# Kernel optimization log

Measured on AMD Instinct MI355X. Metric: run time of the kernel, lower is better.

## Reference

```python
import jax, jax.numpy as jnp
import numpy as np

B = 128
C_IN = 1
HID = 256
LAT = 256
NC = 4096
NA = 16
G = 4
DH = 256        # DynamicsModel default hidden_dim
CE = DH // 2    # code/action embed dim
IMG = 64
COMMIT = 0.25
DN = ('NCHW', 'OIHW', 'NCHW')


def conv_s2(x, w, b):
    y = jax.lax.conv_general_dilated(x, w, (2, 2), ((1, 1), (1, 1)), dimension_numbers=DN)
    return y + b[None, :, None, None]


def deconv_s2(x, w, b):
    # torch ConvTranspose2d(k=4, s=2, p=1): flip kernel, swap I/O channels,
    wt = jnp.flip(w, (2, 3)).transpose(1, 0, 2, 3)
    y = jax.lax.conv_general_dilated(x, wt, (1, 1), ((2, 2), (2, 2)),
                                     lhs_dilation=(2, 2), dimension_numbers=DN)
    return y + b[None, :, None, None]


def setup_inputs():
    key = jax.random.key(0)
    ks = iter(jax.random.split(key, 64))

    def W(shape, fan_in):
        return jax.random.normal(next(ks), shape, jnp.float32) * np.float32(1.0 / np.sqrt(fan_in))

    inp = {}
    inp['x'] = jax.random.uniform(next(ks), (B, C_IN, IMG, IMG), jnp.float32)
    inp['x_next'] = jax.random.uniform(next(ks), (B, C_IN, IMG, IMG), jnp.float32)
    inp['action'] = jax.random.randint(next(ks), (B,), 0, NA)
    # encoder Conv2d weights: [out, in, 4, 4]
    inp['enc_w1'] = W((HID, C_IN, 4, 4), C_IN * 16); inp['enc_b1'] = jnp.zeros((HID,), jnp.float32)
    inp['enc_w2'] = W((HID, HID, 4, 4), HID * 16);   inp['enc_b2'] = jnp.zeros((HID,), jnp.float32)
    inp['enc_w3'] = W((HID, HID, 4, 4), HID * 16);   inp['enc_b3'] = jnp.zeros((HID,), jnp.float32)
    inp['enc_w4'] = W((LAT, HID, 4, 4), HID * 16);   inp['enc_b4'] = jnp.zeros((LAT,), jnp.float32)
    # decoder ConvTranspose2d weights: [in, out, 4, 4]
    inp['dec_w1'] = W((LAT, HID, 4, 4), LAT * 4);    inp['dec_b1'] = jnp.zeros((HID,), jnp.float32)
    inp['dec_w2'] = W((HID, HID, 4, 4), HID * 4);    inp['dec_b2'] = jnp.zeros((HID,), jnp.float32)
    inp['dec_w3'] = W((HID, HID, 4, 4), HID * 4);    inp['dec_b3'] = jnp.zeros((HID,), jnp.float32)
    inp['dec_w4'] = W((HID, C_IN, 4, 4), HID * 4);   inp['dec_b4'] = jnp.zeros((C_IN,), jnp.float32)
    inp['codebook'] = jax.random.normal(next(ks), (NC, LAT), jnp.float32)
    inp['code_embed'] = W((NC, CE), CE)
    inp['action_embed'] = W((NA, CE), CE)
    d_in = G * G * CE + CE
    inp['dyn_w1'] = W((d_in, DH), d_in);      inp['dyn_b1'] = jnp.zeros((DH,), jnp.float32)
    inp['dyn_w2'] = W((DH, DH), DH);          inp['dyn_b2'] = jnp.zeros((DH,), jnp.float32)
    inp['dyn_w3'] = W((DH, G * G * NC), DH);  inp['dyn_b3'] = jnp.zeros((G * G * NC,), jnp.float32)
    return inp


def reference(x, x_next, action,
              enc_w1, enc_b1, enc_w2, enc_b2, enc_w3, enc_b3, enc_w4, enc_b4,
              dec_w1, dec_b1, dec_w2, dec_b2, dec_w3, dec_b3, dec_w4, dec_b4,
              codebook, code_embed, action_embed,
              dyn_w1, dyn_b1, dyn_w2, dyn_b2, dyn_w3, dyn_b3):
    relu = jax.nn.relu
    sg = jax.lax.stop_gradient

    cb_sq = jnp.sum(codebook * codebook, axis=1)  # [NC]

    def encode(xi):
        h = relu(conv_s2(xi, enc_w1, enc_b1))
        h = relu(conv_s2(h, enc_w2, enc_b2))
        h = relu(conv_s2(h, enc_w3, enc_b3))
        z = conv_s2(h, enc_w4, enc_b4)                   # [B, LAT, G, G]
        zf = z.transpose(0, 2, 3, 1).reshape(-1, LAT)    # [B*G*G, LAT]
        # squared euclidean distances (argmin identical to cdist argmin)
        d2 = jnp.sum(zf * zf, axis=1, keepdims=True) - 2.0 * (zf @ codebook.T) + cb_sq
        codes = jnp.argmin(d2, axis=-1)                  # [B*G*G]
        zq = codebook[codes]                             # [B*G*G, LAT]
        return zf, zq, codes

    zf, zq, codes_flat = encode(x)
    commitment_loss = jnp.mean((zf - sg(zq)) ** 2)
    codebook_loss = jnp.mean((sg(zf) - zq) ** 2)
    vq_loss = codebook_loss + COMMIT * commitment_loss
    zq_st = zf + sg(zq - zf)                             # straight-through

    zq_grid = zq_st.reshape(-1, G, G, LAT).transpose(0, 3, 1, 2)  # [B, LAT, G, G]
    codes = codes_flat.reshape(-1, G, G)

    # decoder
    h = relu(deconv_s2(zq_grid, dec_w1, dec_b1))
    h = relu(deconv_s2(h, dec_w2, dec_b2))
    h = relu(deconv_s2(h, dec_w3, dec_b3))
    recon = jax.nn.sigmoid(deconv_s2(h, dec_w4, dec_b4))  # [B, 1, 64, 64]

    # dynamics
    ce = code_embed[codes].reshape(codes.shape[0], -1)    # [B, G*G*CE]
    ae = action_embed[action]                             # [B, CE]
    h2 = jnp.concatenate([ce, ae], axis=-1)
    h2 = relu(h2 @ dyn_w1 + dyn_b1)
    h2 = relu(h2 @ dyn_w2 + dyn_b2)
    next_logits = (h2 @ dyn_w3 + dyn_b3).reshape(-1, G, G, NC)

    # next-code target (no grad in original)
    _, _, nc_flat = encode(sg(x_next))
    next_codes_target = nc_flat.reshape(-1, G, G)

    return (recon, codes, commitment_loss, codebook_loss, vq_loss,
            next_logits, next_codes_target)
```

## Files before the change

### kernel.cpp

```cpp
#include <hip/hip_runtime.h>
#include <hip/hip_bf16.h>

typedef _Float16 f16;
typedef f16   f16x8 __attribute__((ext_vector_type(8)));
typedef short s16x8 __attribute__((ext_vector_type(8)));
typedef float f32x4 __attribute__((ext_vector_type(4)));
typedef unsigned short u16;

__device__ __forceinline__ f32x4 mfma_f16(f16x8 a, f16x8 b, f32x4 c){
  return __builtin_amdgcn_mfma_f32_16x16x32_f16(a,b,c,0,0,0);
}
__device__ __forceinline__ f32x4 mfma_bf16(s16x8 a, s16x8 b, f32x4 c){
  return __builtin_amdgcn_mfma_f32_16x16x32_bf16(a,b,c,0,0,0);
}
__device__ __forceinline__ u16 f2bf(float v){
  unsigned u = __float_as_uint(v);
  unsigned r = u + 0x7fffu + ((u>>16)&1u);
  return (u16)(r>>16);
}
__device__ __forceinline__ float bf2f(u16 v){ return __uint_as_float(((unsigned)v)<<16); }

#define N_B 128

#define OUT_RECON 0
#define OUT_CODES 524288
#define OUT_LC    526336
#define OUT_NL    526339
#define OUT_NCT   8914947

#define B_E1H  0ull
#define B_E1L  67108864ull
#define B_ZF   67108864ull
#define B_ZQ4  69206016ull
#define B_ZSQ  70254592ull
#define B_ACC  70287360ull
#define B_CODES 70320128ull
#define B_H1   70385664ull
#define B_H2   70516736ull
#define B_H2B  70647808ull
#define B_E3H  71303168ull
#define B_E3L  75497472ull
#define B_D1   71303168ull
#define B_D2   75497472ull
#define B_EMB  92274688ull
#define B_ZFH  100663296ull
#define B_ZFL  101711872ull
#define B_E2H  134217728ull
#define B_E2L  150994944ull
#define B_DOTS 134217728ull
#define B_WE2H 167772160ull
#define B_WE2L 169869312ull
#define B_WE3H 171966464ull
#define B_WE3L 174063616ull
#define B_WE4H 176160768ull
#define B_WE4L 178257920ull
#define B_WD1  180355072ull
#define B_WD2  182452224ull
#define B_WD3  184549376ull
#define B_CBSQ 186646528ull
#define B_ZERO 186712064ull
#define B_CBH  186712576ull
#define B_CBL  188809728ull

__global__ __launch_bounds__(256) void k_pack_enc(const float* __restrict__ w,
                                                  f16* __restrict__ Wh, f16* __restrict__ Wl){
  int o = blockIdx.x*256 + threadIdx.x;
  int j=o&7, l=(o>>3)&63, n=(o>>9)&15, icc=(o>>13)&7, tap=o>>16;
  int ic = icc*32 + (l>>4)*8 + j, oc = n*16 + (l&15);
  float v = w[((size_t)oc*256+ic)*16 + tap];
  f16 h = (f16)v;
  Wh[o]=h; Wl[o]=(f16)(v-(float)h);
}
__global__ __launch_bounds__(256) void k_pack_dec(const float* __restrict__ w, u16* __restrict__ Wp){
  int o = blockIdx.x*256 + threadIdx.x;
  int j=o&7, l=(o>>3)&63, n=(o>>9)&15, icc=(o>>13)&7, tap=o>>16;
  int ic = icc*32 + (l>>4)*8 + j, oc = n*16 + (l&15);
  Wp[o] = f2bf(w[((size_t)ic*256+oc)*16 + tap]);
}
__global__ __launch_bounds__(256) void k_pack_cb(const float* __restrict__ cb,
                                                 f16* __restrict__ H, f16* __restrict__ L){
  int s = blockIdx.x*256 + threadIdx.x;
  int n = s>>8, k = s&255;
  float v = cb[s];
  int nt = n>>4, lr2 = n&15, icc = k>>5, rr = k&31, lq2 = rr>>3, j = rr&7;
  size_t o = ((size_t)(nt*8+icc)*64 + lq2*16 + lr2)*8 + j;
  f16 h = (f16)v; H[o]=h; L[o]=(f16)(v-(float)h);
}
__global__ __launch_bounds__(256) void k_cbsq(const float* __restrict__ cb, float* __restrict__ cbsq,
                                              float* __restrict__ zg){
  int c = blockIdx.x*256 + threadIdx.x;
  if(blockIdx.x==0 && threadIdx.x<128) zg[threadIdx.x]=0.f;
  const float4* r4 = (const float4*)(cb + (size_t)c*256);
  float s = 0.f;
  for(int k=0;k<64;k++){ float4 v=r4[k]; s += v.x*v.x+v.y*v.y+v.z*v.z+v.w*v.w; }
  cbsq[c] = s;
}

__global__ __launch_bounds__(256) void k_conv1(const float* __restrict__ x, const float* __restrict__ w1,
                                               const float* __restrict__ b1,
                                               f16* __restrict__ Oh, f16* __restrict__ Ol){
  int b = blockIdx.x >> 5, oy = blockIdx.x & 31;
  int oc = threadIdx.x;
  __shared__ float xs[4][68];
  for(int i=threadIdx.x;i<264;i+=256){
    int rr=i/66, cc=i-rr*66;
    int iy=2*oy-1+rr, ix=cc-1;
    float v=0.f;
    if((unsigned)iy<64u && (unsigned)ix<64u) v = x[((size_t)b*64+iy)*64+ix];
    xs[rr][cc]=v;
  }
  __syncthreads();
  float wv[16];
  #pragma unroll
  for(int k=0;k<16;k++) wv[k]=w1[oc*16+k];
  float bv=b1[oc];
  for(int ox=0;ox<32;ox++){
    float acc=bv;
    int c0=2*ox;
    #pragma unroll
    for(int kh=0;kh<4;kh++)
      #pragma unroll
      for(int kw=0;kw<4;kw++) acc += wv[kh*4+kw]*xs[kh][c0+kw];
    float v = fmaxf(acc,0.f);
    f16 h=(f16)v;
    size_t o = (((size_t)b*32+oy)*32+ox)*256+oc;
    Oh[o]=h; Ol[o]=(f16)(v-(float)h);
  }
}

__global__ __launch_bounds__(512,4) void k_conv_v6(
    const f16* __restrict__ Ah, const f16* __restrict__ Al,
    const f16* __restrict__ Wh, const f16* __restrict__ Wl,
    const float* __restrict__ bias, f16* __restrict__ Oh, f16* __restrict__ Ol){
  constexpr int HIN = 32, HOUT = 16, HH = 256;
  constexpr int ROWS = 64;
  constexpr int IYT = 10, IXT = 34, XS = 40;
  constexpr int RS  = IXT*XS;
  constexpr int BUF = IYT*RS;
  constexpr int ITEMS = IYT*IXT*8;
  __shared__ __align__(16) f16 As[2*BUF];
  const int tid = threadIdx.x, lane = tid&63, w = tid>>6;
  const int wg = w>>2, wn = w&3;
  const int lr = lane&15, lq = lane>>4;
  const int m_base = blockIdx.x*ROWS;
  const int b = m_base/HH;
  const int oy0 = (m_base - b*HH)/HOUT;
  const int iy0 = 2*oy0 - 1;
  const size_t gimg = (size_t)b*HIN*HIN*256;

  int rbw[4];
  #pragma unroll
  for(int t=0;t<4;t++){
    int r = t*16 + lr;
    int oyl = r>>4, oxl = r&15;
    rbw[t] = (2*oyl + 2*wg)*RS + (2*oxl)*XS + lq*8;
  }
  const size_t wgb = (size_t)wg*524288;

  f32x4 acc[4][4];
  #pragma unroll
  for(int t=0;t<4;t++)
    #pragma unroll
    for(int u=0;u<4;u++) acc[t][u] = (f32x4){0.f,0.f,0.f,0.f};

  for(int icc=0;icc<8;icc++){
    __syncthreads();
    for(int s=tid;s<ITEMS;s+=512){
      int c = s&7, posi = s>>3;
      int hl = c>>2, ck = c&3;
      int iyl = posi/IXT, ixl = posi - iyl*IXT;
      int iy = iy0 + iyl, ix = ixl - 1;
      f16x8 v = {0,0,0,0,0,0,0,0};
      if((unsigned)iy<(unsigned)HIN && (unsigned)ix<(unsigned)HIN){
        const f16* src = (hl ? Al : Ah) + gimg + (size_t)(iy*HIN+ix)*256 + icc*32 + ck*8;
        v = *(const f16x8*)src;
      }
      *(f16x8*)&As[hl*BUF + iyl*RS + ixl*XS + ck*8] = v;
    }
    __syncthreads();
    #pragma unroll
    for(int tap8=0;tap8<8;tap8++){
      f16x8 a_h[4], a_l[4];
      #pragma unroll
      for(int t=0;t<4;t++){
        int off = rbw[t] + (tap8>>2)*RS + (tap8&3)*XS;
        a_h[t] = *(const f16x8*)&As[off];
        a_l[t] = *(const f16x8*)&As[BUF + off];
      }
      size_t wb = wgb + ((size_t)(tap8*8+icc)*16 + wn*4)*512 + lane*8;
      #pragma unroll
      for(int u=0;u<4;u++){
        f16x8 b_h = *(const f16x8*)(Wh + wb + u*512);
        f16x8 b_l = *(const f16x8*)(Wl + wb + u*512);
        #pragma unroll
        for(int t=0;t<4;t++){
          acc[t][u] = mfma_f16(a_h[t], b_h, acc[t][u]);
          acc[t][u] = mfma_f16(a_h[t], b_l, acc[t][u]);
          acc[t][u] = mfma_f16(a_l[t], b_h, acc[t][u]);
        }
      }
    }
  }

  float* Rs = (float*)As;
  #pragma unroll
  for(int rr=0;rr<2;rr++){
    __syncthreads();
    if(wg==1){
      #pragma unroll
      for(int t2=0;t2<2;t2++)
        #pragma unroll
        for(int u=0;u<4;u++)
          *(f32x4*)&Rs[((wn*64+lane)*8 + t2*4 + u)*4] = acc[rr*2+t2][u];
    }
    __syncthreads();
    if(wg==0){
      #pragma unroll
      for(int t2=0;t2<2;t2++)
        #pragma unroll
        for(int u=0;u<4;u++){
          f32x4 o = *(const f32x4*)&Rs[((wn*64+lane)*8 + t2*4 + u)*4];
          acc[rr*2+t2][u] += o;
        }
    }
  }
  if(wg==0){
    #pragma unroll
    for(int t=0;t<4;t++){
      #pragma unroll
      for(int u=0;u<4;u++){
        int n = (wn*4+u)*16 + lr;
        float bv = bias[n];
        #pragma unroll
        for(int r=0;r<4;r++){
          int m = m_base + t*16 + lq*4 + r;
          float v = fmaxf(acc[t][u][r] + bv, 0.f);
          size_t o = (size_t)m*256 + n;
          f16 h=(f16)v; Oh[o]=h; Ol[o]=(f16)(v-(float)h);
        }
      }
    }
  }
}

__global__ __launch_bounds__(512,4) void k_conv3_v6(
    const f16* __restrict__ Ah, const f16* __restrict__ Al,
    const f16* __restrict__ Wh, const f16* __restrict__ Wl,
    const float* __restrict__ bias, f16* __restrict__ Oh, f16* __restrict__ Ol){
  constexpr int HIN = 16, HOUT = 8, HH = 64;
  constexpr int ROWS = 16;
  constexpr int IYT = 6, IXT = 18, XS = 40;
  constexpr int RS  = IXT*XS;
  constexpr int BUF = IYT*RS;
  constexpr int ITEMS = IYT*IXT*8;
  __shared__ __align__(16) f16 As[2*BUF];
  const int tid = threadIdx.x, lane = tid&63, w = tid>>6;
  const int wg = w>>2, wn = w&3;
  const int lr = lane&15, lq = lane>>4;
  const int m_base = blockIdx.x*ROWS;
  const int b = m_base/HH;
  const int oy0 = (m_base - b*HH)/HOUT;
  const int iy0 = 2*oy0 - 1;
  const size_t gimg = (size_t)b*HIN*HIN*256;

  const int oyl = lr>>3, oxl = lr&7;
  const int rb = (2*oyl + 2*wg)*RS + (2*oxl)*XS + lq*8;
  const size_t wgb = (size_t)wg*524288;

  f32x4 acc[4];
  #pragma unroll
  for(int u=0;u<4;u++) acc[u] = (f32x4){0.f,0.f,0.f,0.f};

  for(int icc=0;icc<8;icc++){
    __syncthreads();
    for(int s=tid;s<ITEMS;s+=512){
      int c = s&7, posi = s>>3;
      int hl = c>>2, ck = c&3;
      int iyl = posi/IXT, ixl = posi - iyl*IXT;
      int iy = iy0 + iyl, ix = ixl - 1;
      f16x8 v = {0,0,0,0,0,0,0,0};
      if((unsigned)iy<(unsigned)HIN && (unsigned)ix<(unsigned)HIN){
        const f16* src = (hl ? Al : Ah) + gimg + (size_t)(iy*HIN+ix)*256 + icc*32 + ck*8;
        v = *(const f16x8*)src;
      }
      *(f16x8*)&As[hl*BUF + iyl*RS + ixl*XS + ck*8] = v;
    }
    __syncthreads();
    #pragma unroll
    for(int tap8=0;tap8<8;tap8++){
      int off = rb + (tap8>>2)*RS + (tap8&3)*XS;
      f16x8 a_h = *(const f16x8*)&As[off];
      f16x8 a_l = *(const f16x8*)&As[BUF + off];
      size_t wb = wgb + ((size_t)(tap8*8+icc)*16 + wn*4)*512 + lane*8;
      #pragma unroll
      for(int u=0;u<4;u++){
        f16x8 b_h = *(const f16x8*)(Wh + wb + u*512);
        f16x8 b_l = *(const f16x8*)(Wl + wb + u*512);
        acc[u] = mfma_f16(a_h, b_h, acc[u]);
        acc[u] = mfma_f16(a_h, b_l, acc[u]);
        acc[u] = mfma_f16(a_l, b_h, acc[u]);
      }
    }
  }

  f32x4* Rs = (f32x4*)As;
  const int rlane = wn*64 + lane;
  __syncthreads();
  if(wg==1){
    #pragma unroll
    for(int u=0;u<4;u++) Rs[u*256 + rlane] = acc[u];
  }
  __syncthreads();
  if(wg==0){
    #pragma unroll
    for(int u=0;u<4;u++) acc[u] += Rs[u*256 + rlane];
    #pragma unroll
    for(int u=0;u<4;u++){
      int n = (wn*4+u)*16 + lr;
      float bv = bias[n];
      #pragma unroll
      for(int r=0;r<4;r++){
        int m = m_base + lq*4 + r;
        float v = fmaxf(acc[u][r] + bv, 0.f);
        size_t o = (size_t)m*256 + n;
        f16 h=(f16)v; Oh[o]=h; Ol[o]=(f16)(v-(float)h);
      }
    }
  }
}

template<int MT>
__global__ __launch_bounds__(256) void k_conv4(
    const f16* __restrict__ Ah, const f16* __restrict__ Al,
    const f16* __restrict__ Wh, const f16* __restrict__ Wl,
    const float* __restrict__ bias, float* __restrict__ Of,
    f16* __restrict__ Zh, f16* __restrict__ Zl,
    const f16* __restrict__ Zp, int Hin){
  const int Hout = Hin>>1, HH = Hout*Hout;
  const int lane = threadIdx.x & 63, w = threadIdx.x >> 6;
  const int lr = lane & 15, lq = lane >> 4;
  const int m_base = blockIdx.x * (16*MT);
  int iyb[MT], ixb[MT], bb[MT];
  #pragma unroll
  for(int t=0;t<MT;t++){
    int m = m_base + t*16 + lr;
    int b = m/HH, rem = m - b*HH;
    int oy = rem/Hout, ox = rem - oy*Hout;
    bb[t]=b; iyb[t]=2*oy-1; ixb[t]=2*ox-1;
  }
  f32x4 acc[MT][4];
  #pragma unroll
  for(int t=0;t<MT;t++)
    #pragma unroll
    for(int u=0;u<4;u++) acc[t][u]=(f32x4){0.f,0.f,0.f,0.f};

  for(int tap=0;tap<16;tap++){
    int th=tap>>2, tw=tap&3;
    const f16* pH[MT]; const f16* pL[MT];
    #pragma unroll
    for(int t=0;t<MT;t++){
      int iy=iyb[t]+th, ix=ixb[t]+tw;
      bool val = ((unsigned)iy<(unsigned)Hin) && ((unsigned)ix<(unsigned)Hin);
      size_t o = (((size_t)bb[t]*Hin+iy)*Hin+ix)*256 + lq*8;
      pH[t] = val ? Ah+o : Zp;
      pL[t] = val ? Al+o : Zp;
    }
    #pragma unroll
    for(int icc=0;icc<8;icc++){
      f16x8 a_h[MT], a_l[MT];
      #pragma unroll
      for(int t=0;t<MT;t++){
        a_h[t] = *(const f16x8*)(pH[t] + icc*32);
        a_l[t] = *(const f16x8*)(pL[t] + icc*32);
      }
      size_t wb = ((size_t)(tap*8+icc)*16 + w*4)*512 + lane*8;
      #pragma unroll
      for(int u=0;u<4;u++){
        f16x8 b_h = *(const f16x8*)(Wh + wb + u*512);
        f16x8 b_l = *(const f16x8*)(Wl + wb + u*512);
        #pragma unroll
        for(int t=0;t<MT;t++){
          acc[t][u] = mfma_f16(a_h[t], b_h, acc[t][u]);
          acc[t][u] = mfma_f16(a_h[t], b_l, acc[t][u]);
          acc[t][u] = mfma_f16(a_l[t], b_h, acc[t][u]);
        }
      }
    }
  }
  #pragma unroll
  for(int t=0;t<MT;t++){
    #pragma unroll
    for(int u=0;u<4;u++){
      int n = (w*4+u)*16 + lr;
      float bv = bias[n];
      #pragma unroll
      for(int r=0;r<4;r++){
        int m = m_base + t*16 + lq*4 + r;
        float v = acc[t][u][r] + bv;
        size_t o = (size_t)m*256 + n;
        Of[o]=v;
        f16 h=(f16)v; Zh[o]=h; Zl[o]=(f16)(v-(float)h);
      }
    }
  }
}

template<int MT>
__global__ __launch_bounds__(256) void k_deconv_mfma(
    const u16* __restrict__ In, const u16* __restrict__ Wp,
    const float* __restrict__ bias, u16* __restrict__ Out,
    const u16* __restrict__ Zp, int H){
  const int Ho = H*2, HH = H*H;
  const int kh = blockIdx.y>>1, kw = blockIdx.y&1;
  const int lane = threadIdx.x & 63, w = threadIdx.x >> 6;
  const int lr = lane & 15, lq = lane >> 4;
  const int m_base = blockIdx.x * (16*MT);
  int jb[MT], ib[MT], bb[MT];
  #pragma unroll
  for(int t=0;t<MT;t++){
    int m = m_base + t*16 + lr;
    int b = m/HH, rem = m - b*HH;
    jb[t]=rem/H; ib[t]=rem-jb[t]*H; bb[t]=b;
  }
  f32x4 acc[MT][4];
  #pragma unroll
  for(int t=0;t<MT;t++)
    #pragma unroll
    for(int u=0;u<4;u++) acc[t][u]=(f32x4){0.f,0.f,0.f,0.f};

  #pragma unroll
  for(int dy=0;dy<2;dy++){
    #pragma unroll
    for(int dx=0;dx<2;dx++){
      int t16 = (kh+2*dy)*4 + (kw+2*dx);
      const u16* pA[MT];
      #pragma unroll
      for(int t=0;t<MT;t++){
        int r = jb[t]+(1-kh)-dy, c = ib[t]+(1-kw)-dx;
        bool val = ((unsigned)r<(unsigned)H) && ((unsigned)c<(unsigned)H);
        size_t o = (((size_t)bb[t]*H+r)*H+c)*256 + lq*8;
        pA[t] = val ? In+o : Zp;
      }
      #pragma unroll
      for(int icc=0;icc<8;icc++){
        s16x8 a[MT];
        #pragma unroll
        for(int t=0;t<MT;t++) a[t] = *(const s16x8*)(pA[t] + icc*32);
        size_t wb = ((size_t)(t16*8+icc)*16 + w*4)*512 + lane*8;
        #pragma unroll
        for(int u=0;u<4;u++){
          s16x8 bfr = *(const s16x8*)(Wp + wb + u*512);
          #pragma unroll
          for(int t=0;t<MT;t++) acc[t][u] = mfma_bf16(a[t], bfr, acc[t][u]);
        }
      }
    }
  }
  #pragma unroll
  for(int t=0;t<MT;t++){
    #pragma unroll
    for(int u=0;u<4;u++){
      int n = (w*4+u)*16 + lr;
      float bv = bias[n];
      #pragma unroll
      for(int r=0;r<4;r++){
        int m = m_base + t*16 + lq*4 + r;
        int b = m/HH, rem = m - b*HH;
        int j = rem/H, i = rem - j*H;
        int oy = 2*j + (1-kh), ox = 2*i + (1-kw);
        float v = fmaxf(acc[t][u][r] + bv, 0.f);
        Out[(((size_t)b*Ho+oy)*Ho+ox)*256 + n] = f2bf(v);
      }
    }
  }
}

__global__ __launch_bounds__(256) void k_dec4(const u16* __restrict__ In, const float* __restrict__ w4,
                                              const float* __restrict__ bias, float* __restrict__ out){
  __shared__ float wt[16][256];
  int t = threadIdx.x;
  for(int i=t;i<4096;i+=256) wt[i&15][i>>4] = w4[i];
  __syncthreads();
  int ox = t & 63, oy = (blockIdx.x<<2) + (t>>6), b = blockIdx.y;
  int iyh=(oy+1)>>1, kh=(oy+1)&1;
  int ixh=(ox+1)>>1, kw=(ox+1)&1;
  float acc = bias[0];
  #pragma unroll
  for(int dy=0;dy<2;dy++){
    int r = iyh-dy;
    if((unsigned)r>=32u) continue;
    #pragma unroll
    for(int dx=0;dx<2;dx++){
      int c = ixh-dx;
      if((unsigned)c>=32u) continue;
      const u16* p = In + (((size_t)b*32+r)*32+c)*256;
      int widx = (kh+2*dy)*4 + kw+2*dx;
      float s=0.f;
      for(int ic=0;ic<256;ic+=8){
        s16x8 vv = *(const s16x8*)(p+ic);
        const float* wr = &wt[widx][ic];
        #pragma unroll
        for(int q=0;q<8;q++) s += bf2f((u16)vv[q])*wr[q];
      }
      acc += s;
    }
  }
  out[(size_t)b*4096 + oy*64 + ox] = 1.f/(1.f+__expf(-acc));
}

__global__ __launch_bounds__(256) void k_zsq(const float* __restrict__ zf, float* __restrict__ zsq){
  int r=blockIdx.x, c=threadIdx.x;
  float v = zf[(size_t)r*256+c];
  __shared__ float red[256];
  red[c]=v*v; __syncthreads();
  for(int s=128;s>0;s>>=1){ if(c<s) red[c]+=red[c+s]; __syncthreads(); }
  if(c==0) zsq[r]=red[0];
}

__global__ __launch_bounds__(256,2) void k_dots(
    const f16* __restrict__ ZH, const f16* __restrict__ ZL,
    const f16* __restrict__ CH, const f16* __restrict__ CL, float* __restrict__ D){
  const int lane = threadIdx.x & 63, w = threadIdx.x >> 6;
  const int lr = lane & 15, lq = lane >> 4;
  const int m_base = blockIdx.y*64, nb = blockIdx.x;
  f32x4 acc[4][4];
  #pragma unroll
  for(int t=0;t<4;t++)
    #pragma unroll
    for(int u=0;u<4;u++) acc[t][u]=(f32x4){0.f,0.f,0.f,0.f};
  #pragma unroll
  for(int icc=0;icc<8;icc++){
    f16x8 ah[4], al[4];
    #pragma unroll
    for(int t=0;t<4;t++){
      size_t o = (size_t)(m_base + t*16 + lr)*256 + lq*8 + icc*32;
      ah[t] = *(const f16x8*)(ZH+o);
      al[t] = *(const f16x8*)(ZL+o);
    }
    #pragma unroll
    for(int u=0;u<4;u++){
      int nt = nb*16 + w*4 + u;
      size_t wb = ((size_t)(nt*8+icc)*64 + lane)*8;
      f16x8 b_h = *(const f16x8*)(CH+wb);
      f16x8 b_l = *(const f16x8*)(CL+wb);
      #pragma unroll
      for(int t=0;t<4;t++){
        acc[t][u] = mfma_f16(ah[t], b_h, acc[t][u]);
        acc[t][u] = mfma_f16(ah[t], b_l, acc[t][u]);
        acc[t][u] = mfma_f16(al[t], b_h, acc[t][u]);
      }
    }
  }
  #pragma unroll
  for(int t=0;t<4;t++)
    #pragma unroll
    for(int u=0;u<4;u++){
      int n = nb*256 + (w*4+u)*16 + lr;
      #pragma unroll
      for(int r=0;r<4;r++){
        int m = m_base + t*16 + lq*4 + r;
        D[(size_t)m*4096 + n] = acc[t][u][r];
      }
    }
}

__global__ __launch_bounds__(256) void k_argmin(const float* __restrict__ dots, const float* __restrict__ zsq,
                                                const float* __restrict__ cbsq, int* __restrict__ codes,
                                                float* __restrict__ out_codes){
  int r = blockIdx.x, t = threadIdx.x;
  float zs = zsq[r];
  float bv = 1e30f; int bi = 0x7fffffff;
  for(int c=t;c<4096;c+=256){
    float d = zs + cbsq[c] - 2.f*dots[(size_t)r*4096+c];
    if(d < bv || (d==bv && c<bi)){ bv=d; bi=c; }
  }
  __shared__ float sv[256]; __shared__ int si[256];
  sv[t]=bv; si[t]=bi; __syncthreads();
  for(int s=128;s>0;s>>=1){
    if(t<s){
      float v2=sv[t+s]; int i2=si[t+s];
      if(v2<sv[t] || (v2==sv[t] && i2<si[t])){ sv[t]=v2; si[t]=i2; }
    }
    __syncthreads();
  }
  if(t==0){ codes[r]=si[0]; out_codes[r]=(float)si[0]; }
}

__global__ void k_zero(float* a){ a[0]=0.f; }

__global__ __launch_bounds__(256) void k_zqloss(const float* __restrict__ zf, const float* __restrict__ cb,
                                                const int* __restrict__ codes, u16* __restrict__ zq4,
                                                float* __restrict__ accum){
  int r = blockIdx.x, c = threadIdx.x;
  int code = codes[r];
  float q = cb[(size_t)code*256 + c];
  float d = zf[(size_t)r*256+c] - q;
  zq4[(size_t)r*256 + c] = f2bf(q);
  __shared__ float red[256];
  red[c]=d*d; __syncthreads();
  for(int s=128;s>0;s>>=1){ if(c<s) red[c]+=red[c+s]; __syncthreads(); }
  if(c==0) atomicAdd(accum, red[0]);
}

__global__ void k_final(const float* __restrict__ accum, float* __restrict__ out){
  if(threadIdx.x==0){
    float L = accum[0]*(1.f/524288.f);
    out[0]=L; out[1]=L; out[2]=1.25f*L;
  }
}

__global__ __launch_bounds__(256) void k_embed(const int* __restrict__ codes, const int* __restrict__ action,
                                               const float* __restrict__ ce, const float* __restrict__ ae,
                                               float* __restrict__ emb){
  int b = blockIdx.x;
  for(int j=threadIdx.x;j<2176;j+=256){
    float v;
    if(j<2048){ int g=j>>7; v = ce[(size_t)codes[b*16+g]*128 + (j&127)]; }
    else      { v = ae[(size_t)action[b]*128 + (j-2048)]; }
    emb[(size_t)b*2176+j]=v;
  }
}

__global__ __launch_bounds__(256) void k_mlp(const float* __restrict__ in, const float* __restrict__ w,
                                             const float* __restrict__ bias, float* __restrict__ out,
                                             u16* __restrict__ outb, int K){
  int b = blockIdx.x, n = threadIdx.x;
  extern __shared__ float row[];
  for(int k=n;k<K;k+=256) row[k]=in[(size_t)b*K+k];
  __syncthreads();
  float acc = bias[n];
  for(int k=0;k<K;k++) acc += row[k]*w[(size_t)k*256+n];
  float v = fmaxf(acc,0.f);
  out[(size_t)b*256+n] = v;
  if(outb) outb[(size_t)b*256+n] = f2bf(v);
}

__global__ __launch_bounds__(256,2) void k_head(const u16* __restrict__ A,
                                                const float* __restrict__ w3,
                                                const float* __restrict__ b3,
                                                float* __restrict__ O){
  __shared__ u16 BS[8*64*8];
  const int tid = threadIdx.x, lane = tid&63, w = tid>>6;
  const int lr = lane&15, lq = lane>>4;
  const int nb = blockIdx.x;
  f32x4 acc[8][2];
  #pragma unroll
  for(int mt=0;mt<8;mt++)
    #pragma unroll
    for(int u=0;u<2;u++) acc[mt][u]=(f32x4){0.f,0.f,0.f,0.f};
  for(int icc=0;icc<8;icc++){
    __syncthreads();
    #pragma unroll
    for(int q=0;q<4;q++){
      int s = tid*16 + q*4;
      int kl = s>>7, nl = s&127;
      float4 v = *(const float4*)(w3 + (size_t)(icc*32+kl)*65536 + (size_t)nb*128 + nl);
      float vv[4] = {v.x,v.y,v.z,v.w};
      int j = kl&7, lqk = kl>>3;
      #pragma unroll
      for(int e=0;e<4;e++){
        int n2 = nl+e, ntl = n2>>4, lr2 = n2&15;
        BS[(ntl*64 + lqk*16 + lr2)*8 + j] = f2bf(vv[e]);
      }
    }
    __syncthreads();
    s16x8 a[8];
    #pragma unroll
    for(int mt=0;mt<8;mt++)
      a[mt] = *(const s16x8*)(A + (size_t)(mt*16+lr)*256 + icc*32 + lq*8);
    #pragma unroll
    for(int u=0;u<2;u++){
      int ntl = w*2+u;
      s16x8 bfr = *(const s16x8*)&BS[((size_t)ntl*64 + lane)*8];
      #pragma unroll
      for(int mt=0;mt<8;mt++) acc[mt][u] = mfma_bf16(a[mt], bfr, acc[mt][u]);
    }
  }
  #pragma unroll
  for(int mt=0;mt<8;mt++)
    #pragma unroll
    for(int u=0;u<2;u++){
      int n = nb*128 + (w*2+u)*16 + lr;
      float bv = b3[n];
      #pragma unroll
      for(int r=0;r<4;r++){
        int m = mt*16 + lq*4 + r;
        O[(size_t)m*65536 + n] = acc[mt][u][r] + bv;
      }
    }
}

extern "C" void kernel_launch(void* const* d_in, const int* in_sizes, int n_in,
                              void* d_out, int out_size, void* d_ws, size_t ws_size,
                              hipStream_t stream){
  (void)in_sizes; (void)n_in; (void)out_size; (void)ws_size;
  const float* x    = (const float*)d_in[0];
  const float* xn   = (const float*)d_in[1];
  const int*   act  = (const int*)  d_in[2];
  const float* ew1=(const float*)d_in[3];  const float* eb1=(const float*)d_in[4];
  const float* ew2=(const float*)d_in[5];  const float* eb2=(const float*)d_in[6];
  const float* ew3=(const float*)d_in[7];  const float* eb3=(const float*)d_in[8];
  const float* ew4=(const float*)d_in[9];  const float* eb4=(const float*)d_in[10];
  const float* dw1=(const float*)d_in[11]; const float* db1=(const float*)d_in[12];
  const float* dw2=(const float*)d_in[13]; const float* db2=(const float*)d_in[14];
  const float* dw3=(const float*)d_in[15]; const float* db3=(const float*)d_in[16];
  const float* dw4=(const float*)d_in[17]; const float* db4=(const float*)d_in[18];
  const float* cbk =(const float*)d_in[19];
  const float* cemb=(const float*)d_in[20];
  const float* aemb=(const float*)d_in[21];
  const float* yw1=(const float*)d_in[22]; const float* yb1=(const float*)d_in[23];
  const float* yw2=(const float*)d_in[24]; const float* yb2=(const float*)d_in[25];
  const float* yw3=(const float*)d_in[26]; const float* yb3=(const float*)d_in[27];
  float* out = (float*)d_out;

  char* wsb = (char*)d_ws;
  f16* E1H=(f16*)(wsb+B_E1H); f16* E1L=(f16*)(wsb+B_E1L);
  f16* E2H=(f16*)(wsb+B_E2H); f16* E2L=(f16*)(wsb+B_E2L);
  f16* E3H=(f16*)(wsb+B_E3H); f16* E3L=(f16*)(wsb+B_E3L);
  float* ZF=(float*)(wsb+B_ZF);
  f16* ZFH=(f16*)(wsb+B_ZFH); f16* ZFL=(f16*)(wsb+B_ZFL);
  u16* ZQ4=(u16*)(wsb+B_ZQ4);
  f16* WE2H=(f16*)(wsb+B_WE2H); f16* WE2L=(f16*)(wsb+B_WE2L);
  f16* WE3H=(f16*)(wsb+B_WE3H); f16* WE3L=(f16*)(wsb+B_WE3L);
  f16* WE4H=(f16*)(wsb+B_WE4H); f16* WE4L=(f16*)(wsb+B_WE4L);
  u16* WD1=(u16*)(wsb+B_WD1); u16* WD2=(u16*)(wsb+B_WD2); u16* WD3=(u16*)(wsb+B_WD3);
  f16* CBH=(f16*)(wsb+B_CBH); f16* CBL=(f16*)(wsb+B_CBL);
  float* ZSQ=(float*)(wsb+B_ZSQ); float* CBSQ=(float*)(wsb+B_CBSQ);
  float* EMB=(float*)(wsb+B_EMB); float* H1=(float*)(wsb+B_H1); float* H2=(float*)(wsb+B_H2);
  u16* H2B=(u16*)(wsb+B_H2B);
  float* ACC=(float*)(wsb+B_ACC); int* CODES=(int*)(wsb+B_CODES);
  float* ZG=(float*)(wsb+B_ZERO);
  const f16* Zf16=(const f16*)ZG; const u16* Zbf=(const u16*)ZG;
  float* DOTS=(float*)(wsb+B_DOTS);
  u16* D1=(u16*)(wsb+B_D1);
  u16* D2=(u16*)(wsb+B_D2);
  u16* D3=(u16*)(wsb+B_E1H);

  k_pack_enc<<<4096,256,0,stream>>>(ew2, WE2H, WE2L);
  k_pack_enc<<<4096,256,0,stream>>>(ew3, WE3H, WE3L);
  k_pack_enc<<<4096,256,0,stream>>>(ew4, WE4H, WE4L);
  k_pack_dec<<<4096,256,0,stream>>>(dw1, WD1);
  k_pack_dec<<<4096,256,0,stream>>>(dw2, WD2);
  k_pack_dec<<<4096,256,0,stream>>>(dw3, WD3);
  k_pack_cb <<<4096,256,0,stream>>>(cbk, CBH, CBL);
  k_cbsq<<<16,256,0,stream>>>(cbk, CBSQ, ZG);

  auto encode = [&](const float* img, float* code_out){
    k_conv1<<<4096,256,0,stream>>>(img, ew1, eb1, E1H, E1L);
    k_conv_v6<<<512,512,0,stream>>>(E1H,E1L, WE2H,WE2L, eb2, E2H,E2L);
    k_conv3_v6<<<512,512,0,stream>>>(E2H,E2L, WE3H,WE3L, eb3, E3H,E3L);
    k_conv4<1><<<128,256,0,stream>>>(E3H,E3L, WE4H,WE4L, eb4, ZF, ZFH, ZFL, Zf16, 8);
    k_zsq<<<2048,256,0,stream>>>(ZF, ZSQ);
    k_dots<<<dim3(16,32),256,0,stream>>>(ZFH, ZFL, CBH, CBL, DOTS);
    k_argmin<<<2048,256,0,stream>>>(DOTS, ZSQ, CBSQ, CODES, code_out);
  };

  encode(x, out+OUT_CODES);
  k_zero<<<1,1,0,stream>>>(ACC);
  k_zqloss<<<2048,256,0,stream>>>(ZF, cbk, CODES, ZQ4, ACC);
  k_final<<<1,64,0,stream>>>(ACC, out+OUT_LC);

  k_deconv_mfma<1><<<dim3(128,4),256,0,stream>>>(ZQ4, WD1, db1, D1, Zbf, 4);
  k_deconv_mfma<4><<<dim3(128,4),256,0,stream>>>(D1,  WD2, db2, D2, Zbf, 8);
  k_deconv_mfma<4><<<dim3(512,4),256,0,stream>>>(D2,  WD3, db3, D3, Zbf, 16);
  k_dec4<<<dim3(16,N_B),256,0,stream>>>(D3, dw4, db4, out+OUT_RECON);

  k_embed<<<N_B,256,0,stream>>>(CODES, act, cemb, aemb, EMB);
  k_mlp<<<N_B,256,2176*4,stream>>>(EMB, yw1, yb1, H1, nullptr, 2176);
  k_mlp<<<N_B,256, 256*4,stream>>>(H1,  yw2, yb2, H2, H2B, 256);
  k_head<<<512,256,0,stream>>>(H2B, yw3, yb3, out+OUT_NL);

  encode(xn, out+OUT_NCT);
}
```

Measured before the change: 1.746 ms.

## Split conv4 across channel halves and tap groups; use nontemporal conv2/3 loads and stores

The last encoder conv is rewritten from 128 blocks of 256 threads into 256 blocks of 512 threads. Each block covers half the output channels, and its two wave groups each handle half of the 16 taps, with partial sums reduced through shared memory. The goal is to expose more parallelism for a small-M GEMM that underfilled the GPU, at the cost of extra shared-memory reduction and synchronisation. The conv2/conv3 input loads and output stores are also switched to nontemporal builtins to reduce cache pollution, which may hurt if those activations would have been reused from cache by the next kernel.

Result: faster. 1.631 ms (-6.6%).

```diff
diff --git a/kernel.cpp b/kernel.cpp
--- a/kernel.cpp
+++ b/kernel.cpp
@@ -173,7 +173,7 @@
       f16x8 v = {0,0,0,0,0,0,0,0};
       if((unsigned)iy<(unsigned)HIN && (unsigned)ix<(unsigned)HIN){
         const f16* src = (hl ? Al : Ah) + gimg + (size_t)(iy*HIN+ix)*256 + icc*32 + ck*8;
-        v = *(const f16x8*)src;
+        v = __builtin_nontemporal_load((const f16x8*)src);
       }
       *(f16x8*)&As[hl*BUF + iyl*RS + ixl*XS + ck*8] = v;
     }
@@ -236,7 +236,9 @@
           int m = m_base + t*16 + lq*4 + r;
           float v = fmaxf(acc[t][u][r] + bv, 0.f);
           size_t o = (size_t)m*256 + n;
-          f16 h=(f16)v; Oh[o]=h; Ol[o]=(f16)(v-(float)h);
+          f16 h=(f16)v;
+          __builtin_nontemporal_store(h, &Oh[o]);
+          __builtin_nontemporal_store((f16)(v-(float)h), &Ol[o]);
         }
       }
     }
@@ -281,7 +283,7 @@
       f16x8 v = {0,0,0,0,0,0,0,0};
       if((unsigned)iy<(unsigned)HIN && (unsigned)ix<(unsigned)HIN){
         const f16* src = (hl ? Al : Ah) + gimg + (size_t)(iy*HIN+ix)*256 + icc*32 + ck*8;
-        v = *(const f16x8*)src;
+        v = __builtin_nontemporal_load((const f16x8*)src);
       }
       *(f16x8*)&As[hl*BUF + iyl*RS + ixl*XS + ck*8] = v;
     }
@@ -323,81 +325,79 @@
         int m = m_base + lq*4 + r;
         float v = fmaxf(acc[u][r] + bv, 0.f);
         size_t o = (size_t)m*256 + n;
-        f16 h=(f16)v; Oh[o]=h; Ol[o]=(f16)(v-(float)h);
-      }
-    }
-  }
-}
-
-template<int MT>
-__global__ __launch_bounds__(256) void k_conv4(
+        f16 h=(f16)v;
+        __builtin_nontemporal_store(h, &Oh[o]);
+        __builtin_nontemporal_store((f16)(v-(float)h), &Ol[o]);
+      }
+    }
+  }
+}
+
+__global__ __launch_bounds__(512,4) void k_conv4_v6(
     const f16* __restrict__ Ah, const f16* __restrict__ Al,
     const f16* __restrict__ Wh, const f16* __restrict__ Wl,
     const float* __restrict__ bias, float* __restrict__ Of,
     f16* __restrict__ Zh, f16* __restrict__ Zl,
-    const f16* __restrict__ Zp, int Hin){
-  const int Hout = Hin>>1, HH = Hout*Hout;
-  const int lane = threadIdx.x & 63, w = threadIdx.x >> 6;
-  const int lr = lane & 15, lq = lane >> 4;
-  const int m_base = blockIdx.x * (16*MT);
-  int iyb[MT], ixb[MT], bb[MT];
-  #pragma unroll
-  for(int t=0;t<MT;t++){
-    int m = m_base + t*16 + lr;
-    int b = m/HH, rem = m - b*HH;
-    int oy = rem/Hout, ox = rem - oy*Hout;
-    bb[t]=b; iyb[t]=2*oy-1; ixb[t]=2*ox-1;
-  }
-  f32x4 acc[MT][4];
-  #pragma unroll
-  for(int t=0;t<MT;t++)
-    #pragma unroll
-    for(int u=0;u<4;u++) acc[t][u]=(f32x4){0.f,0.f,0.f,0.f};
-
-  for(int tap=0;tap<16;tap++){
-    int th=tap>>2, tw=tap&3;
-    const f16* pH[MT]; const f16* pL[MT];
-    #pragma unroll
-    for(int t=0;t<MT;t++){
-      int iy=iyb[t]+th, ix=ixb[t]+tw;
-      bool val = ((unsigned)iy<(unsigned)Hin) && ((unsigned)ix<(unsigned)Hin);
-      size_t o = (((size_t)bb[t]*Hin+iy)*Hin+ix)*256 + lq*8;
-      pH[t] = val ? Ah+o : Zp;
-      pL[t] = val ? Al+o : Zp;
-    }
+    const f16* __restrict__ Zp){
+  constexpr int HIN = 8, HOUT = 4, HH = 16;
+  __shared__ f32x4 Red[512];
+  const int tid = threadIdx.x, lane = tid&63, w = tid>>6;
+  const int wg = w>>2, wn = w&3;
+  const int lr = lane&15, lq = lane>>4;
+  const int mt = blockIdx.x;
+  const int ny = blockIdx.y;
+  const int m = mt*16 + lr;
+  const int b = m>>4, rem = m&15;
+  const int oy = rem>>2, ox = rem&3;
+  const int iyb = 2*oy-1, ixb = 2*ox-1;
+
+  f32x4 acc[2];
+  acc[0]=(f32x4){0.f,0.f,0.f,0.f}; acc[1]=(f32x4){0.f,0.f,0.f,0.f};
+
+  #pragma unroll
+  for(int tap8=0;tap8<8;tap8++){
+    const int tap = wg*8 + tap8;
+    const int th = tap>>2, tw = tap&3;
+    int iy = iyb+th, ix = ixb+tw;
+    bool val = ((unsigned)iy<(unsigned)HIN) && ((unsigned)ix<(unsigned)HIN);
+    size_t o = (((size_t)b*HIN+iy)*HIN+ix)*256 + lq*8;
+    const f16* pH = val ? Ah+o : Zp;
+    const f16* pL = val ? Al+o : Zp;
     #pragma unroll
     for(int icc=0;icc<8;icc++){
-      f16x8 a_h[MT], a_l[MT];
-      #pragma unroll
-      for(int t=0;t<MT;t++){
-        a_h[t] = *(const f16x8*)(pH[t] + icc*32);
-        a_l[t] = *(const f16x8*)(pL[t] + icc*32);
-      }
-      size_t wb = ((size_t)(tap*8+icc)*16 + w*4)*512 + lane*8;
-      #pragma unroll
-      for(int u=0;u<4;u++){
+      f16x8 a_h = *(const f16x8*)(pH + icc*32);
+      f16x8 a_l = *(const f16x8*)(pL + icc*32);
+      size_t wb = ((size_t)(tap*8+icc)*16 + ny*8 + wn*2)*512 + lane*8;
+      #pragma unroll
+      for(int u=0;u<2;u++){
         f16x8 b_h = *(const f16x8*)(Wh + wb + u*512);
         f16x8 b_l = *(const f16x8*)(Wl + wb + u*512);
-        #pragma unroll
-        for(int t=0;t<MT;t++){
-          acc[t][u] = mfma_f16(a_h[t], b_h, acc[t][u]);
-          acc[t][u] = mfma_f16(a_h[t], b_l, acc[t][u]);
-          acc[t][u] = mfma_f16(a_l[t], b_h, acc[t][u]);
-        }
-      }
-    }
-  }
-  #pragma unroll
-  for(int t=0;t<MT;t++){
-    #pragma unroll
-    for(int u=0;u<4;u++){
-      int n = (w*4+u)*16 + lr;
+        acc[u] = mfma_f16(a_h, b_h, acc[u]);
+        acc[u] = mfma_f16(a_h, b_l, acc[u]);
+        acc[u] = mfma_f16(a_l, b_h, acc[u]);
+      }
+    }
+  }
+
+  const int rl = wn*64 + lane;
+  __syncthreads();
+  if(wg==1){
+    Red[0*256+rl] = acc[0];
+    Red[1*256+rl] = acc[1];
+  }
+  __syncthreads();
+  if(wg==0){
+    acc[0] += Red[0*256+rl];
+    acc[1] += Red[1*256+rl];
+    #pragma unroll
+    for(int u=0;u<2;u++){
+      int n = ny*128 + (wn*2+u)*16 + lr;
       float bv = bias[n];
       #pragma unroll
       for(int r=0;r<4;r++){
-        int m = m_base + t*16 + lq*4 + r;
-        float v = acc[t][u][r] + bv;
-        size_t o = (size_t)m*256 + n;
+        int m2 = mt*16 + lq*4 + r;
+        float v = acc[u][r] + bv;
+        size_t o = (size_t)m2*256 + n;
         Of[o]=v;
         f16 h=(f16)v; Zh[o]=h; Zl[o]=(f16)(v-(float)h);
       }
@@ -749,7 +749,7 @@
     k_conv1<<<4096,256,0,stream>>>(img, ew1, eb1, E1H, E1L);
     k_conv_v6<<<512,512,0,stream>>>(E1H,E1L, WE2H,WE2L, eb2, E2H,E2L);
     k_conv3_v6<<<512,512,0,stream>>>(E2H,E2L, WE3H,WE3L, eb3, E3H,E3L);
-    k_conv4<1><<<128,256,0,stream>>>(E3H,E3L, WE4H,WE4L, eb4, ZF, ZFH, ZFL, Zf16, 8);
+    k_conv4_v6<<<dim3(128,2),512,0,stream>>>(E3H,E3L, WE4H,WE4L, eb4, ZF, ZFH, ZFL, Zf16);
     k_zsq<<<2048,256,0,stream>>>(ZF, ZSQ);
     k_dots<<<dim3(16,32),256,0,stream>>>(ZFH, ZFL, CBH, CBL, DOTS);
     k_argmin<<<2048,256,0,stream>>>(DOTS, ZSQ, CBSQ, CODES, code_out);
```
